# Kernel optimization log

Measured on AMD Instinct MI355X. Metric: run time of the kernel, lower is better.

## Reference

```python
import jax, jax.numpy as jnp
import numpy as np

SQN = 3      # hardcoded recurrence depth
ATT_H = 256  # hardcoded attention hidden size
STRIDE = 16  # segment length (hardcoded expand(-1,16,-1))


def setup_inputs() -> dict:
    key = jax.random.key(0)
    ks = jax.random.split(key, 12)
    B, Cin, H, V = 64, 512, 512, 512

    def w(k, shape, fan_in):
        return jax.random.normal(k, shape, jnp.float32) / np.sqrt(fan_in).astype(np.float32)

    return {
        "visual_input": jax.random.normal(ks[0], (B, Cin, V), jnp.float32),
        "text_feature": jax.random.normal(ks[1], (B, H), jnp.float32),
        # weights stored [in, out] (transposed vs torch nn.Linear)
        "vis_conv_w": w(ks[2], (Cin, H), Cin),   # 1x1 Conv1d == linear over channels
        "vis_conv_b": jnp.zeros((H,), jnp.float32),
        "glob_w": w(ks[3], (SQN, H, H), H),      # 3 distinct global_emb linears
        "glob_b": jnp.zeros((SQN, H), jnp.float32),
        "guide_w": w(ks[4], (2 * H, H), 2 * H),
        "guide_b": jnp.zeros((H,), jnp.float32),
        "att1_w": w(ks[5], (H, ATT_H), H),
        "att1_b": jnp.zeros((ATT_H,), jnp.float32),
        "att2_w": w(ks[6], (H, ATT_H), H),
        "att2_b": jnp.zeros((ATT_H,), jnp.float32),
        "att3_w": w(ks[7], (ATT_H, 1), ATT_H),
        "att3_b": jnp.zeros((1,), jnp.float32),
        "out_conv_w": w(ks[8], (H, H), H),       # 1x1 Conv1d
        "out_conv_b": jnp.zeros((H,), jnp.float32),
        "text_w": w(ks[9], (H, H), H),
        "text_b": jnp.zeros((H,), jnp.float32),
    }


def reference(visual_input, text_feature, vis_conv_w, vis_conv_b, glob_w, glob_b,
              guide_w, guide_b, att1_w, att1_b, att2_w, att2_b, att3_w, att3_b,
              out_conv_w, out_conv_b, text_w, text_b):
    B, Cin, V = visual_input.shape
    H = vis_conv_w.shape[1]
    S = V // STRIDE  # number of segments

    # vis_conv (1x1) + relu: [B, H, V]
    vis_h = jax.nn.relu(jnp.einsum('bcv,ch->bhv', visual_input, vis_conv_w)
                        + vis_conv_b[None, :, None])
    # split into segments: [B, S, T=16, H]
    vis_seg = vis_h.reshape(B, H, S, STRIDE).transpose(0, 2, 3, 1)
    # AvgPool1d(kernel=stride) == per-segment mean: [B, S, H]
    avg_seg = vis_seg.mean(axis=2)
    # text projection: [B, H]
    text_att = text_feature @ text_w + text_b

    # precompute att_fn2(vis_seg): [B, S, T, ATT_H] (loop-invariant)
    att2_pre = jnp.einsum('bsth,ha->bsta', vis_seg, att2_w) + att2_b

    prev_se = jnp.zeros((B, S, H), vis_seg.dtype)
    se_list, att_list = [], []
    for m in range(SQN):  # fixed 3-step recurrence, distinct weights per step
        v_n = jnp.einsum('bsh,hk->bsk', avg_seg, glob_w[m]) + glob_b[m]
        # guide_emb (Linear+ReLU) followed by an outer relu == single relu
        g_n = jax.nn.relu(jnp.concatenate([v_n, prev_se], axis=-1) @ guide_w + guide_b)
        att = jnp.tanh((g_n @ att1_w + att1_b)[:, :, None, :] + att2_pre)  # [B,S,T,A]
        att = att @ att3_w + att3_b                                        # [B,S,T,1]
        att = jax.nn.softmax(att, axis=2)  # softmax over the 16 frames
        prev_se = jnp.sum(vis_seg * att, axis=2)  # [B, S, H]
        se_list.append(prev_se)
        att_list.append(att)

    vis_for_att = jnp.stack(se_list, axis=2)  # [B, S, 3, H]
    fuse_att = jax.nn.softmax(jnp.einsum('bsmh,bh->bsm', vis_for_att, text_att), axis=2)
    vis_new = jnp.einsum('bsmh,bsm->bsh', vis_for_att, fuse_att)  # [B, S, H]

    # vis_out_conv (1x1) + relu over stacked segments: [B, H, S]
    vis_out = jax.nn.relu(jnp.einsum('bsh,hk->bks', vis_new, out_conv_w)
                          + out_conv_b[None, :, None])
    att_out = jnp.concatenate(att_list, axis=3)  # [B, S, 16, 3]
    return vis_out, att_out
```

## Files before the change

### kernel.cpp

```cpp
#include <hip/hip_runtime.h>

#define B_   64
#define CIN_ 512
#define H_   512
#define V_   512
#define S_   32
#define T_   16
#define A_   256
#define SQN_ 3
#define BS_  2048

typedef float  f32x4  __attribute__((ext_vector_type(4)));
typedef float  f32x2  __attribute__((ext_vector_type(2)));
typedef short  short8 __attribute__((ext_vector_type(8)));
typedef short  short4v __attribute__((ext_vector_type(4)));
typedef unsigned int uint4v __attribute__((ext_vector_type(4)));

__device__ __forceinline__ unsigned short f2bf(float f) {
    union { float f; unsigned int u; } v; v.f = f;
    unsigned int u = v.u;
    unsigned int r = (u + 0x7fffu + ((u >> 16) & 1u)) >> 16;
    return (unsigned short)r;
}
__device__ __forceinline__ float bf2f(unsigned short h) {
    union { unsigned int u; float f; } v; v.u = ((unsigned int)h) << 16;
    return v.f;
}

__device__ __forceinline__ float fast_tanhf(float x) {
    float cx = fminf(fmaxf(x, -15.0f), 15.0f);
    float e  = __expf(2.0f * cx);
    return (e - 1.0f) * __builtin_amdgcn_rcpf(e + 1.0f);
}

__device__ __forceinline__ void gload16(const void* g, void* l) {
    __builtin_amdgcn_global_load_lds(
        (const __attribute__((address_space(1))) unsigned int*)g,
        (__attribute__((address_space(3))) unsigned int*)l,
        16, 0, 0);
}

template <int N> __device__ __forceinline__ void waitv() {
    asm volatile("s_waitcnt vmcnt(%0)" :: "n"(N) : "memory");
}

__global__ __launch_bounds__(256) void prep_kernel(
    const float* __restrict__ visual, const float* __restrict__ vis_conv_w,
    const float* __restrict__ att2_w, const float* __restrict__ guide_w,
    const float* __restrict__ att1_w, const float* __restrict__ out_conv_w,
    const float* __restrict__ glob_w, const float* __restrict__ text_feature,
    const float* __restrict__ text_w, const float* __restrict__ text_b,
    const float* __restrict__ glob_b, const float* __restrict__ guide_b,
    unsigned short* __restrict__ visT, unsigned short* __restrict__ wT_visconv,
    unsigned short* __restrict__ wT_att2, unsigned short* __restrict__ wT_guide,
    unsigned short* __restrict__ wT_att1, unsigned short* __restrict__ wT_out,
    unsigned short* __restrict__ glob_bf, float* __restrict__ text_part,
    float* __restrict__ bcomb)
{
    __shared__ __align__(16) char smem[32768];
    const int id  = blockIdx.x;
    const int tid = threadIdx.x;

    if (id < 128) {
        const int nt = id & 7, kc = id >> 3;
        const int n0 = nt * 64, kbase = kc * 32;
        float* Ts = (float*)smem;
        float* Ws = (float*)smem + 64 * 33;
        {
            const int m = tid >> 2, kk = (tid & 3) * 8;
            #pragma unroll
            for (int c = 0; c < 8; c += 4)
                *(f32x4*)&Ts[m * 33 + kk + c] =
                    *(const f32x4*)&text_feature[m * 512 + kbase + kk + c];
            const int kr = tid >> 3, nn = (tid & 7) * 8;
            #pragma unroll
            for (int c = 0; c < 8; c += 4)
                *(f32x4*)&Ws[kr * 65 + nn + c] =
                    *(const f32x4*)&text_w[(long long)(kbase + kr) * 512 + n0 + nn + c];
        }
        __syncthreads();
        const int tm = (tid >> 4) * 4, tn = (tid & 15) * 4;
        float acc[4][4] = {};
        for (int k = 0; k < 32; k++) {
            float a[4], b2[4];
            #pragma unroll
            for (int i = 0; i < 4; i++) a[i] = Ts[(tm + i) * 33 + k];
            #pragma unroll
            for (int j = 0; j < 4; j++) b2[j] = Ws[k * 65 + tn + j];
            #pragma unroll
            for (int i = 0; i < 4; i++)
                #pragma unroll
                for (int j = 0; j < 4; j++) acc[i][j] += a[i] * b2[j];
        }
        #pragma unroll
        for (int i = 0; i < 4; i++)
            #pragma unroll
            for (int j = 0; j < 4; j++)
                text_part[kc * (64 * 512) + (tm + i) * 512 + n0 + tn + j] =
                    acc[i][j] + (kc == 0 ? text_b[n0 + tn + j] : 0.0f);
        return;
    }
    if (id < 131) {
        const int m = id - 128;
        const int j2 = tid * 2;
        float a0 = guide_b[j2], a1 = guide_b[j2 + 1];
        const float* gb = glob_b + m * 512;
        #pragma unroll 8
        for (int k = 0; k < 512; k++) {
            const float g = gb[k];
            f32x2 w = *(const f32x2*)&guide_w[(long long)k * 512 + j2];
            a0 += g * w[0];
            a1 += g * w[1];
        }
        f32x2 o = {a0, a1};
        *(f32x2*)&bcomb[m * 512 + j2] = o;
        return;
    }
    if (id < 227) {
        const int base = (id - 131) * 8192 + tid * 4;
        #pragma unroll
        for (int it = 0; it < 8; it++) {
            f32x4 v = *(const f32x4*)&glob_w[base + it * 1024];
            short4v o;
            #pragma unroll
            for (int c = 0; c < 4; c++) o[c] = (short)f2bf(v[c]);
            *(short4v*)&glob_bf[base + it * 1024] = o;
        }
        return;
    }

    if (id >= 547) {
        const int q = id - 547;
        const int b = q >> 5, tile = q & 31;
        const int k0 = (tile >> 2) << 6;
        const int v0 = (tile & 3) << 7;
        const float* src = visual + (long long)b * 262144;
        unsigned short* dst = visT + (long long)b * 262144;
        float* tl = (float*)smem;

        const int wave = tid >> 6, lane = tid & 63;
        #pragma unroll
        for (int i = 0; i < 8; i++) {
            const int r2 = wave * 16 + i * 2;
            gload16(&src[(long long)(k0 + r2 + (lane >> 5)) * 512 + v0 + (lane & 31) * 4],
                    &tl[r2 * 128]);
        }
        __syncthreads();

        const int kl = (tid & 7) * 8;
        const int vb = tid >> 3;
        #pragma unroll
        for (int jv = 0; jv < 4; jv++) {
            const int v = vb + jv * 32;
            short8 o;
            #pragma unroll
            for (int i = 0; i < 8; i++)
                o[i] = (short)f2bf(tl[(kl + i) * 128 + v]);
            *(short8*)&dst[(long long)(v0 + v) * 512 + k0 + kl] = o;
        }
        return;
    }

    const float* src; unsigned short* dst; int Kd, Nd, tile;
    if (id < 291)      { tile = id - 227; src = vis_conv_w; dst = wT_visconv; Kd = 512;  Nd = 512; }
    else if (id < 323) { tile = id - 291; src = att2_w;     dst = wT_att2;    Kd = 512;  Nd = 256; }
    else if (id < 451) { tile = id - 323; src = guide_w;    dst = wT_guide;   Kd = 1024; Nd = 512; }
    else if (id < 483) { tile = id - 451; src = att1_w;     dst = wT_att1;    Kd = 512;  Nd = 256; }
    else               { tile = id - 483; src = out_conv_w; dst = wT_out;     Kd = 512;  Nd = 512; }

    unsigned int* tl = (unsigned int*)smem;
    const int xw = Nd >> 6;
    const int n0 = (tile % xw) << 6, k0 = (tile / xw) << 6;
    {
        const int r = tid >> 4;
        const int c4 = (tid & 15) * 4;
        #pragma unroll
        for (int j = 0; j < 4; j++) {
            const int row = j * 16 + r;
            f32x4 v = *(const f32x4*)&src[(long long)(k0 + row) * Nd + n0 + c4];
            #pragma unroll
            for (int c2 = 0; c2 < 4; c2++)
                tl[row * 65 + c4 + c2] = f2bf(v[c2]);
        }
    }
    __syncthreads();
    {
        const int v = tid >> 2, cq = (tid & 3) * 16;
        short8 o0, o1;
        #pragma unroll
        for (int j = 0; j < 8; j++) o0[j] = (short)tl[(cq + j) * 65 + v];
        #pragma unroll
        for (int j = 0; j < 8; j++) o1[j] = (short)tl[(cq + 8 + j) * 65 + v];
        *(short8*)&dst[(long long)(n0 + v) * Kd + k0 + cq] = o0;
        *(short8*)&dst[(long long)(n0 + v) * Kd + k0 + cq + 8] = o1;
    }
}

template <int BM, int BN, bool RELU, bool OUT_BF16, int OUT_MODE, bool ACC_INIT, int DEPTH>
__device__ __forceinline__ void gemm_body(
    char* pool, int bid, int nwg,
    const unsigned short* __restrict__ A, long long aBatch, int lda,
    const unsigned short* __restrict__ Bt, long long bBatch, int ldb,
    const float* __restrict__ bias, long long biasBatch,
    const float* __restrict__ Cinit, int ldci,
    void* __restrict__ C, long long cBatch, int ldc,
    void* __restrict__ C2, unsigned short* __restrict__ avg_out,
    int M, int N, int K)
{
    constexpr int WM = BM / 2, WN = BN / 2;
    constexpr int FI = WM / 16, FJ = WN / 16;
    constexpr int LOADS = BM / 64 + BN / 64;
    constexpr bool CT_EN  = (OUT_MODE != 1);
    constexpr bool CT_F32 = CT_EN && ((OUT_MODE == 0 && !OUT_BF16) || OUT_MODE == 3);
    constexpr int  CTS    = CT_F32 ? (BN + 4) : (BN + 8);
    constexpr int  KLOOP_B = DEPTH * (BM * 32 + BN * 32) * 2;
    constexpr int  CT_B    = CT_EN ? (BM * CTS * (CT_F32 ? 4 : 2)) : 0;
    constexpr int  MAIN_B  = (KLOOP_B > CT_B ? KLOOP_B : CT_B);
    unsigned short* As = (unsigned short*)pool;
    unsigned short* Bs = As + DEPTH * BM * 32;
    float* avgl = (float*)(pool + MAIN_B);

    const int q8 = nwg >> 3, r8 = nwg & 7;
    const int xcd = bid & 7, lid = bid >> 3;
    const int logical = (xcd < r8 ? xcd * (q8 + 1)
                                  : r8 * (q8 + 1) + (xcd - r8) * q8) + lid;

    const int ntiles = N / BN;
    const int tilesPerBatch = (M / BM) * ntiles;
    const int batch = logical / tilesPerBatch;
    const int t     = logical % tilesPerBatch;
    const int tm0 = (t / ntiles) * BM;
    const int tn0 = (t % ntiles) * BN;
    const unsigned short* Ab = A + (long long)batch * aBatch;
    const unsigned short* Bb = Bt + (long long)batch * bBatch;

    const int tid  = threadIdx.x;
    const int lane = tid & 63;
    const int wave = tid >> 6;
    const int wm = (wave >> 1) * WM;
    const int wn = (wave & 1) * WN;
    const int lr = lane & 15;
    const int lk = (lane >> 4) * 8;
    const int rsub = lane >> 2;
    const int g8s = ((lane & 3) ^ ((lane >> 3) & 3)) * 8;
    const int lks = lk ^ (((lr >> 1) & 3) << 3);

    auto stage = [&](int buf, int k0) {
        #pragma unroll
        for (int i = 0; i < BM / 64; i++) {
            const int rbase = wave * (BM / 4) + i * 16;
            gload16(&Ab[(long long)(tm0 + rbase + rsub) * lda + k0 + g8s],
                    &As[buf * (BM * 32) + rbase * 32]);
        }
        #pragma unroll
        for (int i = 0; i < BN / 64; i++) {
            const int rbase = wave * (BN / 4) + i * 16;
            gload16(&Bb[(long long)(tn0 + rbase + rsub) * ldb + k0 + g8s],
                    &Bs[buf * (BN * 32) + rbase * 32]);
        }
    };

    f32x4 acc[FI][FJ] = {};
    const int nk = K >> 5;

    #pragma unroll
    for (int d = 0; d < DEPTH - 1; d++)
        if (d < nk) stage(d, d << 5);

    int cur = 0;
    for (int kt = 0; kt < nk; kt++) {
        if (kt + DEPTH - 1 < nk) {
            const int nb = cur + DEPTH - 1;
            stage(nb >= DEPTH ? nb - DEPTH : nb, (kt + DEPTH - 1) << 5);
        }
        if constexpr (DEPTH == 2) {
            if (kt + 1 < nk) waitv<LOADS>(); else waitv<0>();
        } else {
            if (kt + 2 < nk)      waitv<2 * LOADS>();
            else if (kt + 1 < nk) waitv<LOADS>();
            else                  waitv<0>();
        }
        __builtin_amdgcn_s_barrier();

        const unsigned short* Ac = As + cur * (BM * 32);
        const unsigned short* Bc = Bs + cur * (BN * 32);
        short8 a[FI], b[FJ];
        #pragma unroll
        for (int i = 0; i < FI; i++)
            a[i] = *(const short8*)&Ac[(wm + i * 16 + lr) * 32 + lks];
        #pragma unroll
        for (int j = 0; j < FJ; j++)
            b[j] = *(const short8*)&Bc[(wn + j * 16 + lr) * 32 + lks];
        #pragma unroll
        for (int i = 0; i < FI; i++)
            #pragma unroll
            for (int j = 0; j < FJ; j++)
                acc[i][j] = __builtin_amdgcn_mfma_f32_16x16x32_bf16(
                    a[i], b[j], acc[i][j], 0, 0, 0);
        __builtin_amdgcn_sched_barrier(0);
        __builtin_amdgcn_s_barrier();
        cur = (cur + 1 == DEPTH) ? 0 : cur + 1;
    }

    const int erow = (lane >> 4) * 4;
    const int ecol = lane & 15;

    if constexpr (OUT_MODE == 1) {
        #pragma unroll
        for (int i = 0; i < FI; i++) {
            #pragma unroll
            for (int j = 0; j < FJ; j++) {
                const int gcol = tn0 + wn + j * 16 + ecol;
                const float bv = bias ? bias[gcol] : 0.0f;
                const int grow0 = tm0 + wm + i * 16 + erow;
                const int bb = grow0 >> 5, ss = grow0 & 31;
                f32x4 o;
                #pragma unroll
                for (int r = 0; r < 4; r++) o[r] = fmaxf(acc[i][j][r] + bv, 0.0f);
                *(f32x4*)&((float*)C)[(long long)bb * (H_ * S_) + gcol * S_ + ss] = o;
            }
        }
        return;
    } else {
        __syncthreads();
        unsigned short* CTh = (unsigned short*)pool;
        float*          CTf = (float*)pool;

        #pragma unroll
        for (int i = 0; i < FI; i++) {
            #pragma unroll
            for (int j = 0; j < FJ; j++) {
                const int lcol = wn + j * 16 + ecol;
                const int gcol = tn0 + lcol;
                const float bv = bias ? bias[(long long)batch * biasBatch + gcol] : 0.0f;
                float csum = 0.0f;
                #pragma unroll
                for (int r = 0; r < 4; r++) {
                    const int lrow = wm + i * 16 + erow + r;
                    float v = acc[i][j][r] + bv;
                    if (ACC_INIT) v += Cinit[(long long)(tm0 + lrow) * ldci + gcol];
                    if (RELU) v = fmaxf(v, 0.0f);
                    if constexpr (CT_F32) CTf[lrow * CTS + lcol] = v;
                    else                  CTh[lrow * CTS + lcol] = f2bf(v);
                    if constexpr (OUT_MODE == 2) csum += v;
                }
                if constexpr (OUT_MODE == 2) {
                    csum += __shfl_xor(csum, 16, 64);
                    csum += __shfl_xor(csum, 32, 64);
                    if (lane < 16)
                        avgl[((wm >> 4) + i) * BN + wn + j * 16 + lane] = csum;
                }
            }
        }
        __syncthreads();

        if constexpr (CT_F32) {
            constexpr int ITERS = (BM * BN) / 1024;
            #pragma unroll
            for (int it = 0; it < ITERS; it++) {
                const int flat = it * 1024 + tid * 4;
                const int row = flat / BN, col = flat % BN;
                f32x4 vv = *(const f32x4*)&CTf[row * CTS + col];
                if constexpr (OUT_MODE == 3) {
                    if (batch == 0) {
                        short4v p;
                        #pragma unroll
                        for (int c = 0; c < 4; c++) p[c] = (short)f2bf(fmaxf(vv[c], 0.0f));
                        *(short4v*)&((unsigned short*)C2)[(long long)(tm0 + row) * ldc + tn0 + col] = p;
                    } else {
                        *(f32x4*)&((float*)C)[(long long)(batch - 1) * cBatch +
                                              (long long)(tm0 + row) * ldc + tn0 + col] = vv;
                    }
                } else {
                    *(f32x4*)&((float*)C)[(long long)batch * cBatch +
                                          (long long)(tm0 + row) * ldc + tn0 + col] = vv;
                }
            }
        } else {
            constexpr int ITERS = (BM * BN) / 2048;
            #pragma unroll
            for (int it = 0; it < ITERS; it++) {
                const int flat = it * 2048 + tid * 8;
                const int row = flat / BN, col = flat % BN;
                short8 vv = *(const short8*)&CTh[row * CTS + col];
                *(short8*)&((unsigned short*)C)[(long long)batch * cBatch +
                                                (long long)(tm0 + row) * ldc + tn0 + col] = vv;
            }
        }

        if constexpr (OUT_MODE == 2) {
            const int s = tid >> 5, hq = (tid & 31) * 4;
            short4v pk;
            #pragma unroll
            for (int c = 0; c < 4; c++)
                pk[c] = (short)f2bf(avgl[s * BN + hq + c] * (1.0f / 16.0f));
            *(short4v*)&avg_out[((long long)batch * 32 + (tm0 >> 4) + s) * H_ + tn0 + hq] = pk;
        }
    }
}

__device__ __forceinline__ void visconv_pair_body(
    char* pool, int bid, int nwg,
    const unsigned short* __restrict__ visT,
    const unsigned short* __restrict__ Bw,
    const float* __restrict__ bias,
    unsigned short* __restrict__ vis_seg,
    unsigned short* __restrict__ avg_out)
{
    unsigned short* As = (unsigned short*)pool;
    unsigned short* Bs = As + 16384;
    float* avgl = (float*)(pool + 49152);

    const int logical = (bid & 7) * (nwg >> 3) + (bid >> 3);
    const int pairIdx = logical >> 4;
    const int t = logical & 15;
    const int tm0 = (t >> 2) * 128, tn0 = (t & 3) * 128;
    const int b0 = pairIdx * 2;
    const unsigned short* A0 = visT + (long long)b0 * (V_ * CIN_);
    const unsigned short* A1 = A0 + V_ * CIN_;

    const int tid  = threadIdx.x;
    const int lane = tid & 63, wave = tid >> 6;
    const int wm = (wave >> 1) * 64, wn = (wave & 1) * 64;
    const int lr = lane & 15, lk = (lane >> 4) * 8;
    const int rsub = lane >> 2;
    const int g8s = ((lane & 3) ^ ((lane >> 3) & 3)) * 8;
    const int lks = lk ^ (((lr >> 1) & 3) << 3);

    auto stage = [&](int buf, int k0) {
        #pragma unroll
        for (int i = 0; i < 2; i++) {
            const int rbase = wave * 32 + i * 16;
            gload16(&A0[(long long)(tm0 + rbase + rsub) * CIN_ + k0 + g8s],
                    &As[(0 + buf) * 4096 + rbase * 32]);
            gload16(&A1[(long long)(tm0 + rbase + rsub) * CIN_ + k0 + g8s],
                    &As[(2 + buf) * 4096 + rbase * 32]);
            gload16(&Bw[(long long)(tn0 + rbase + rsub) * CIN_ + k0 + g8s],
                    &Bs[buf * 4096 + rbase * 32]);
        }
    };

    f32x4 acc0[4][4] = {}, acc1[4][4] = {};

    stage(0, 0);
    int cur = 0;
    for (int kt = 0; kt < 16; kt++) {
        if (kt + 1 < 16) stage(cur ^ 1, (kt + 1) << 5);
        if (kt + 1 < 16) waitv<6>(); else waitv<0>();
        __builtin_amdgcn_s_barrier();

        const unsigned short* Bc = Bs + cur * 4096;
        short8 b[4];
        #pragma unroll
        for (int j = 0; j < 4; j++)
            b[j] = *(const short8*)&Bc[(wn + j * 16 + lr) * 32 + lks];
        {
            const unsigned short* Ac = As + cur * 4096;
            short8 a[4];
            #pragma unroll
            for (int i = 0; i < 4; i++)
                a[i] = *(const short8*)&Ac[(wm + i * 16 + lr) * 32 + lks];
            #pragma unroll
            for (int i = 0; i < 4; i++)
                #pragma unroll
                for (int j = 0; j < 4; j++)
                    acc0[i][j] = __builtin_amdgcn_mfma_f32_16x16x32_bf16(
                        a[i], b[j], acc0[i][j], 0, 0, 0);
        }
        {
            const unsigned short* Ac = As + (2 + cur) * 4096;
            short8 a[4];
            #pragma unroll
            for (int i = 0; i < 4; i++)
                a[i] = *(const short8*)&Ac[(wm + i * 16 + lr) * 32 + lks];
            #pragma unroll
            for (int i = 0; i < 4; i++)
                #pragma unroll
                for (int j = 0; j < 4; j++)
                    acc1[i][j] = __builtin_amdgcn_mfma_f32_16x16x32_bf16(
                        a[i], b[j], acc1[i][j], 0, 0, 0);
        }
        __builtin_amdgcn_sched_barrier(0);
        __builtin_amdgcn_s_barrier();
        cur ^= 1;
    }

    const int erow = (lane >> 4) * 4;
    const int ecol = lane & 15;
    unsigned short* CTh = (unsigned short*)pool;

    auto epil = [&](f32x4 (&acc)[4][4], int b) {
        #pragma unroll
        for (int i = 0; i < 4; i++) {
            #pragma unroll
            for (int j = 0; j < 4; j++) {
                const int lcol = wn + j * 16 + ecol;
                const float bv = bias[tn0 + lcol];
                float csum = 0.0f;
                #pragma unroll
                for (int r = 0; r < 4; r++) {
                    const int lrow = wm + i * 16 + erow + r;
                    float v = fmaxf(acc[i][j][r] + bv, 0.0f);
                    CTh[lrow * 136 + lcol] = f2bf(v);
                    csum += v;
                }
                csum += __shfl_xor(csum, 16, 64);
                csum += __shfl_xor(csum, 32, 64);
                if (lane < 16)
                    avgl[((wm >> 4) + i) * 128 + wn + j * 16 + lane] = csum;
            }
        }
        __syncthreads();
        #pragma unroll
        for (int it = 0; it < 8; it++) {
            const int flat = it * 2048 + tid * 8;
            const int row = flat >> 7, col = flat & 127;
            short8 vv = *(const short8*)&CTh[row * 136 + col];
            *(short8*)&vis_seg[(long long)b * (V_ * H_) +
                               (long long)(tm0 + row) * H_ + tn0 + col] = vv;
        }
        {
            const int s = tid >> 5, hq = (tid & 31) * 4;
            short4v pk;
            #pragma unroll
            for (int c = 0; c < 4; c++)
                pk[c] = (short)f2bf(avgl[s * 128 + hq + c] * (1.0f / 16.0f));
            *(short4v*)&avg_out[((long long)b * 32 + (tm0 >> 4) + s) * H_ + tn0 + hq] = pk;
        }
        __syncthreads();
    };
    epil(acc0, b0);
    epil(acc1, b0 + 1);
}

template <int BM, int BN, bool RELU, bool OUT_BF16, int OUT_MODE, bool ACC_INIT, int DEPTH>
__global__ __launch_bounds__(256) void mfma_gemm(
    const unsigned short* A, long long aBatch, int lda,
    const unsigned short* Bt, long long bBatch, int ldb,
    const float* bias, long long biasBatch,
    const float* Cinit, int ldci,
    void* C, long long cBatch, int ldc,
    void* C2, unsigned short* avg_out,
    int M, int N, int K)
{
    constexpr bool CT_EN  = (OUT_MODE != 1);
    constexpr bool CT_F32 = CT_EN && ((OUT_MODE == 0 && !OUT_BF16) || OUT_MODE == 3);
    constexpr int  CTS    = CT_F32 ? (BN + 4) : (BN + 8);
    constexpr int  KLOOP_B = DEPTH * (BM * 32 + BN * 32) * 2;
    constexpr int  CT_B    = CT_EN ? (BM * CTS * (CT_F32 ? 4 : 2)) : 0;
    constexpr int  MAIN_B  = (KLOOP_B > CT_B ? KLOOP_B : CT_B);
    constexpr int  AVG_B   = (OUT_MODE == 2) ? (BM / 16) * BN * 4 : 0;
    __shared__ __align__(16) char pool[MAIN_B + AVG_B];
    gemm_body<BM, BN, RELU, OUT_BF16, OUT_MODE, ACC_INIT, DEPTH>(
        pool, blockIdx.x, gridDim.x,
        A, aBatch, lda, Bt, bBatch, ldb, bias, biasBatch, Cinit, ldci,
        C, cBatch, ldc, C2, avg_out, M, N, K);
}

__global__ __launch_bounds__(256) void wcomb_visconv_kernel(
    const unsigned short* wT_guide, const unsigned short* glob_bf,
    unsigned short* WcombT,
    const unsigned short* visT, const unsigned short* wT_visconv,
    const float* vis_conv_b, unsigned short* vis_seg, unsigned short* avg)
{
    __shared__ __align__(16) char pool[53248];
    if (blockIdx.x < 192) {
        gemm_body<64, 64, false, true, 0, false, 2>(pool, blockIdx.x, 192,
            wT_guide, 0, 1024,
            glob_bf, (long long)H_ * H_, H_,
            nullptr, 0, nullptr, 0,
            WcombT, (long long)H_ * H_, H_, nullptr, nullptr, H_, H_, H_);
    } else {
        visconv_pair_body(pool, blockIdx.x - 192, 512,
            visT, wT_visconv, vis_conv_b, vis_seg, avg);
    }
}

__global__ __launch_bounds__(256) void att2_p_kernel(
    const unsigned short* vis_seg, const unsigned short* wT_att2,
    const float* att2_b, unsigned short* att2_pre,
    const unsigned short* avg, const unsigned short* WcombT,
    const float* bcomb, float* P, unsigned short* gbuf)
{
    __shared__ __align__(16) char pool[34816];
    if (blockIdx.x < 512) {
        gemm_body<128, 128, false, true, 0, false, 2>(pool, blockIdx.x, 512,
            vis_seg, (long long)V_ * H_, H_,
            wT_att2, 0, H_,
            att2_b, 0, nullptr, 0,
            att2_pre, (long long)V_ * A_, A_, nullptr, nullptr, V_, A_, H_);
    } else {
        gemm_body<64, 64, false, false, 3, false, 2>(pool, blockIdx.x - 512, 768,
            avg, 0, H_,
            WcombT, (long long)H_ * H_, H_,
            bcomb, H_, nullptr, 0,
            P, (long long)BS_ * H_, H_, gbuf, nullptr, BS_, H_, H_);
    }
}

template <bool LAST>
__global__ __launch_bounds__(256) void fused_att_kernel(
    const float* __restrict__ att1,
    const unsigned short* __restrict__ att2_pre,
    const float* __restrict__ att3_w,
    const float* __restrict__ att3_b,
    const unsigned short* __restrict__ vis_seg,
    float* __restrict__ se_m,
    unsigned short* __restrict__ pse,
    float* __restrict__ att_out, int m,
    const float* __restrict__ se_base,
    const float* __restrict__ text_part,
    const float* __restrict__ text_b,
    unsigned short* __restrict__ vis_new)
{
    const int bs = blockIdx.x, tid = threadIdx.x;
    const int wave = tid >> 6, lane = tid & 63;
    __shared__ float logits[T_], wts[T_];
    __shared__ float part[3][512];
    __shared__ float redf[4][3];
    __shared__ float swf[3];
    __shared__ float tsh[512];

    if constexpr (LAST) {
        const int b = bs >> 5;
        for (int h = tid; h < 512; h += 256) {
            float s = text_b[h];
            #pragma unroll
            for (int p = 0; p < 16; p++)
                s += text_part[p * (64 * 512) + b * 512 + h];
            tsh[h] = s;
        }
    }

    f32x4 a1r = *(const f32x4*)&att1[(long long)bs * A_ + lane * 4];
    f32x4 w3r = *(const f32x4*)&att3_w[lane * 4];

    #pragma unroll
    for (int qq = 0; qq < 4; qq++) {
        const int t = wave * 4 + qq;
        short4v ap = *(const short4v*)&att2_pre[(long long)(bs * T_ + t) * A_ + lane * 4];
        float x = 0.f;
        #pragma unroll
        for (int c = 0; c < 4; c++)
            x += fast_tanhf(a1r[c] + bf2f((unsigned short)ap[c])) * w3r[c];
        #pragma unroll
        for (int off = 32; off > 0; off >>= 1) x += __shfl_down(x, off, 64);
        if (lane == 0) logits[t] = x + att3_b[0];
    }
    __syncthreads();
    if (tid == 0) {
        float mx = logits[0];
        #pragma unroll
        for (int t = 1; t < T_; t++) mx = fmaxf(mx, logits[t]);
        float s = 0.f;
        #pragma unroll
        for (int t = 0; t < T_; t++) { float e = expf(logits[t] - mx); wts[t] = e; s += e; }
        float inv = 1.0f / s;
        #pragma unroll
        for (int t = 0; t < T_; t++) wts[t] *= inv;
    }
    __syncthreads();
    if (tid < T_) att_out[bs * (T_ * SQN_) + tid * SQN_ + m] = wts[tid];

    const int slot = tid & 63, quarter = tid >> 6;
    float s[8] = {};
    #pragma unroll
    for (int tt = 0; tt < 4; tt++) {
        const int t = quarter * 4 + tt;
        short8 vv = *(const short8*)&vis_seg[(long long)(bs * T_ + t) * H_ + slot * 8];
        const float w = wts[t];
        #pragma unroll
        for (int c = 0; c < 8; c++) s[c] += bf2f((unsigned short)vv[c]) * w;
    }
    if (quarter) {
        #pragma unroll
        for (int c = 0; c < 8; c++) part[quarter - 1][slot * 8 + c] = s[c];
    }
    __syncthreads();
    if (quarter == 0) {
        #pragma unroll
        for (int c = 0; c < 8; c++)
            s[c] += part[0][slot * 8 + c] + part[1][slot * 8 + c] + part[2][slot * 8 + c];
    }

    if constexpr (!LAST) {
        if (quarter == 0) {
            f32x4 o0 = {s[0], s[1], s[2], s[3]};
            f32x4 o1 = {s[4], s[5], s[6], s[7]};
            *(f32x4*)&se_m[(long long)bs * H_ + slot * 8] = o0;
            *(f32x4*)&se_m[(long long)bs * H_ + slot * 8 + 4] = o1;
            short8 p;
            #pragma unroll
            for (int c = 0; c < 8; c++) p[c] = (short)f2bf(s[c]);
            *(short8*)&pse[(long long)bs * H_ + slot * 8] = p;
        }
    } else {
        const float* se0 = se_base + (long long)bs * H_;
        const float* se1 = se_base + (long long)BS_ * H_ + (long long)bs * H_;

        float p0 = 0.f, p1 = 0.f, p2 = 0.f;
        {
            const int h2 = tid * 2;
            float t0 = tsh[h2], t1 = tsh[h2 + 1];
            p0 = se0[h2] * t0 + se0[h2 + 1] * t1;
            p1 = se1[h2] * t0 + se1[h2 + 1] * t1;
        }
        if (quarter == 0) {
            #pragma unroll
            for (int c = 0; c < 8; c++) p2 += s[c] * tsh[slot * 8 + c];
        }
        #pragma unroll
        for (int off = 32; off > 0; off >>= 1) {
            p0 += __shfl_down(p0, off, 64);
            p1 += __shfl_down(p1, off, 64);
            p2 += __shfl_down(p2, off, 64);
        }
        if (lane == 0) { redf[wave][0] = p0; redf[wave][1] = p1; redf[wave][2] = p2; }
        __syncthreads();
        if (tid == 0) {
            float d0 = redf[0][0] + redf[1][0] + redf[2][0] + redf[3][0];
            float d1 = redf[0][1] + redf[1][1] + redf[2][1] + redf[3][1];
            float d2 = redf[0][2] + redf[1][2] + redf[2][2] + redf[3][2];
            float mx = fmaxf(d0, fmaxf(d1, d2));
            float e0 = expf(d0 - mx), e1 = expf(d1 - mx), e2 = expf(d2 - mx);
            float inv = 1.0f / (e0 + e1 + e2);
            swf[0] = e0 * inv; swf[1] = e1 * inv; swf[2] = e2 * inv;
        }
        __syncthreads();
        if (quarter == 0) {
            const float w0 = swf[0], w1 = swf[1], w2 = swf[2];
            short8 p;
            #pragma unroll
            for (int c = 0; c < 8; c++) {
                const int h = slot * 8 + c;
                p[c] = (short)f2bf(w0 * se0[h] + w1 * se1[h] + w2 * s[c]);
            }
            *(short8*)&vis_new[(long long)bs * H_ + slot * 8] = p;
        }
    }
}

extern "C" void kernel_launch(void* const* d_in, const int* in_sizes, int n_in,
                              void* d_out, int out_size, void* d_ws, size_t ws_size,
                              hipStream_t stream)
{
    const float* visual       = (const float*)d_in[0];
    const float* text_feature = (const float*)d_in[1];
    const float* vis_conv_w   = (const float*)d_in[2];
    const float* vis_conv_b   = (const float*)d_in[3];
    const float* glob_w       = (const float*)d_in[4];
    const float* glob_b       = (const float*)d_in[5];
    const float* guide_w      = (const float*)d_in[6];
    const float* guide_b      = (const float*)d_in[7];
    const float* att1_w       = (const float*)d_in[8];
    const float* att1_b       = (const float*)d_in[9];
    const float* att2_w       = (const float*)d_in[10];
    const float* att2_b       = (const float*)d_in[11];
    const float* att3_w       = (const float*)d_in[12];
    const float* att3_b       = (const float*)d_in[13];
    const float* out_conv_w   = (const float*)d_in[14];
    const float* out_conv_b   = (const float*)d_in[15];
    const float* text_w       = (const float*)d_in[16];
    const float* text_b       = (const float*)d_in[17];
    float* out = (float*)d_out;
    float* att_out = out + (B_ * H_ * S_);

    char* base = (char*)d_ws;
    unsigned short* visT     = (unsigned short*)(base + 0);
    unsigned short* vis_seg  = (unsigned short*)(base + 33554432);
    unsigned short* att2_pre = (unsigned short*)(base + 67108864);
    float*          se       = (float*)(base + 100663296);
    float*          P        = (float*)(base + 113246208);
    unsigned short* pse      = (unsigned short*)(base + 125829120);
    unsigned short* gbuf     = (unsigned short*)(base + 127926272);
    float*          att1buf  = (float*)(base + 130023424);
    unsigned short* avg      = (unsigned short*)(base + 132120576);
    unsigned short* vis_new  = (unsigned short*)(base + 134348800);
    char*           wbase    = base + 136445952;
    unsigned short* wT_visconv = (unsigned short*)(wbase + 0);
    unsigned short* wT_att2    = (unsigned short*)(wbase + 524288);
    unsigned short* wT_guide   = (unsigned short*)(wbase + 786432);
    unsigned short* wT_att1    = (unsigned short*)(wbase + 1835008);
    unsigned short* wT_out     = (unsigned short*)(wbase + 2097152);
    unsigned short* glob_bf    = (unsigned short*)(wbase + 2621440);
    unsigned short* WcombT     = (unsigned short*)(wbase + 4194304);
    float*          bcomb      = (float*)(wbase + 5767168);
    float*          text_part  = (float*)(wbase + 6291456);

    prep_kernel<<<dim3(2595), 256, 0, stream>>>(
        visual, vis_conv_w, att2_w, guide_w, att1_w, out_conv_w, glob_w,
        text_feature, text_w, text_b, glob_b, guide_b,
        visT, wT_visconv, wT_att2, wT_guide, wT_att1, wT_out,
        glob_bf, text_part, bcomb);

    wcomb_visconv_kernel<<<dim3(192 + 512), 256, 0, stream>>>(
        wT_guide, glob_bf, WcombT,
        visT, wT_visconv, vis_conv_b, vis_seg, avg);

    att2_p_kernel<<<dim3(512 + 768), 256, 0, stream>>>(
        vis_seg, wT_att2, att2_b, att2_pre,
        avg, WcombT, bcomb, P, gbuf);

    for (int m = 0; m < SQN_; m++) {
        if (m > 0) {
            mfma_gemm<64, 64, true, true, 0, true, 3><<<dim3(256), 256, 0, stream>>>(
                pse, 0, H_,
                wT_guide + 512, 0, 1024,
                nullptr, 0, P + (long long)(m - 1) * BS_ * H_, H_,
                gbuf, 0, H_, nullptr, nullptr, BS_, H_, H_);
        }
        mfma_gemm<64, 64, false, false, 0, false, 3><<<dim3(128), 256, 0, stream>>>(
            gbuf, 0, H_,
            wT_att1, 0, H_,
            att1_b, 0, nullptr, 0,
            att1buf, 0, A_, nullptr, nullptr, BS_, A_, H_);
        if (m < SQN_ - 1) {
            fused_att_kernel<false><<<dim3(BS_), 256, 0, stream>>>(
                att1buf, att2_pre, att3_w, att3_b, vis_seg,
                se + (long long)m * BS_ * H_, pse, att_out, m,
                nullptr, nullptr, nullptr, nullptr);
        } else {
            fused_att_kernel<true><<<dim3(BS_), 256, 0, stream>>>(
                att1buf, att2_pre, att3_w, att3_b, vis_seg,
                nullptr, nullptr, att_out, m,
                se, text_part, text_b, vis_new);
        }
    }

    mfma_gemm<64, 64, true, false, 1, false, 3><<<dim3(256), 256, 0, stream>>>(
        vis_new, 0, H_,
        wT_out, 0, H_,
        out_conv_b, 0, nullptr, 0,
        out, 0, 0, nullptr, nullptr, BS_, H_, H_);
}
```

Baseline: 164.8 us.

## Fuse visual input transpose and bf16 cast into vis_conv GEMM A-loading

Drops the prep-kernel pass that transposed the fp32 visual input into a bf16 visT buffer. The vis_conv GEMM now stages fp32 tiles of the visual input straight into LDS, using an XOR swizzle, and converts them to bf16 when building the MFMA A fragments. Each block now handles one batch instead of a pair, so the grid doubles and the shared B tile is no longer reused across two batches. This removes a 64MB read and 32MB write round trip, but the GEMM now reads fp32 A (twice the bytes), does scalar strided LDS reads, and spends extra ALU on conversion in the inner loop.

Measured after the change: 176.5 us. 7.1% more time.

```diff
diff --git a/kernel.cpp b/kernel.cpp
--- a/kernel.cpp
+++ b/kernel.cpp
@@ -45,13 +45,13 @@
 }
 
 __global__ __launch_bounds__(256) void prep_kernel(
-    const float* __restrict__ visual, const float* __restrict__ vis_conv_w,
+    const float* __restrict__ vis_conv_w,
     const float* __restrict__ att2_w, const float* __restrict__ guide_w,
     const float* __restrict__ att1_w, const float* __restrict__ out_conv_w,
     const float* __restrict__ glob_w, const float* __restrict__ text_feature,
     const float* __restrict__ text_w, const float* __restrict__ text_b,
     const float* __restrict__ glob_b, const float* __restrict__ guide_b,
-    unsigned short* __restrict__ visT, unsigned short* __restrict__ wT_visconv,
+    unsigned short* __restrict__ wT_visconv,
     unsigned short* __restrict__ wT_att2, unsigned short* __restrict__ wT_guide,
     unsigned short* __restrict__ wT_att1, unsigned short* __restrict__ wT_out,
     unsigned short* __restrict__ glob_bf, float* __restrict__ text_part,
@@ -125,38 +125,6 @@
             #pragma unroll
             for (int c = 0; c < 4; c++) o[c] = (short)f2bf(v[c]);
             *(short4v*)&glob_bf[base + it * 1024] = o;
-        }
-        return;
-    }
-
-    if (id >= 547) {
-        const int q = id - 547;
-        const int b = q >> 5, tile = q & 31;
-        const int k0 = (tile >> 2) << 6;
-        const int v0 = (tile & 3) << 7;
-        const float* src = visual + (long long)b * 262144;
-        unsigned short* dst = visT + (long long)b * 262144;
-        float* tl = (float*)smem;
-
-        const int wave = tid >> 6, lane = tid & 63;
-        #pragma unroll
-        for (int i = 0; i < 8; i++) {
-            const int r2 = wave * 16 + i * 2;
-            gload16(&src[(long long)(k0 + r2 + (lane >> 5)) * 512 + v0 + (lane & 31) * 4],
-                    &tl[r2 * 128]);
-        }
-        __syncthreads();
-
-        const int kl = (tid & 7) * 8;
-        const int vb = tid >> 3;
-        #pragma unroll
-        for (int jv = 0; jv < 4; jv++) {
-            const int v = vb + jv * 32;
-            short8 o;
-            #pragma unroll
-            for (int i = 0; i < 8; i++)
-                o[i] = (short)f2bf(tl[(kl + i) * 128 + v]);
-            *(short8*)&dst[(long long)(v0 + v) * 512 + k0 + kl] = o;
         }
         return;
     }
@@ -399,49 +367,49 @@
     }
 }
 
-__device__ __forceinline__ void visconv_pair_body(
+__device__ __forceinline__ void visconv_f32_body(
     char* pool, int bid, int nwg,
-    const unsigned short* __restrict__ visT,
+    const float* __restrict__ visual,
     const unsigned short* __restrict__ Bw,
     const float* __restrict__ bias,
     unsigned short* __restrict__ vis_seg,
     unsigned short* __restrict__ avg_out)
 {
-    unsigned short* As = (unsigned short*)pool;
-    unsigned short* Bs = As + 16384;
-    float* avgl = (float*)(pool + 49152);
+    float*          Asf = (float*)pool;
+    unsigned short* Bs  = (unsigned short*)(pool + 32768);
+    float*          avgl = (float*)(pool + 49152);
 
     const int logical = (bid & 7) * (nwg >> 3) + (bid >> 3);
-    const int pairIdx = logical >> 4;
+    const int b = logical >> 4;
     const int t = logical & 15;
-    const int tm0 = (t >> 2) * 128, tn0 = (t & 3) * 128;
-    const int b0 = pairIdx * 2;
-    const unsigned short* A0 = visT + (long long)b0 * (V_ * CIN_);
-    const unsigned short* A1 = A0 + V_ * CIN_;
-
-    const int tid  = threadIdx.x;
-    const int lane = tid & 63, wave = tid >> 6;
+    const int tm0 = (t >> 2) * 128;
+    const int tn0 = (t & 3) * 128;
+    const float* Ab = visual + (long long)b * (CIN_ * V_);
+
+    const int tid = threadIdx.x, lane = tid & 63, wave = tid >> 6;
     const int wm = (wave >> 1) * 64, wn = (wave & 1) * 64;
     const int lr = lane & 15, lk = (lane >> 4) * 8;
     const int rsub = lane >> 2;
     const int g8s = ((lane & 3) ^ ((lane >> 3) & 3)) * 8;
     const int lks = lk ^ (((lr >> 1) & 3) << 3);
+    const int vsrc = ((lane & 31) * 4) ^ ((wave & 1) << 4);
+    const int akey = ((lane >> 4) & 1) << 4;
 
     auto stage = [&](int buf, int k0) {
+        #pragma unroll
+        for (int i = 0; i < 4; i++) {
+            gload16(&Ab[(long long)(k0 + wave * 8 + i * 2 + (lane >> 5)) * V_ + tm0 + vsrc],
+                    (char*)Asf + buf * 16384 + (wave * 8 + i * 2) * 512);
+        }
         #pragma unroll
         for (int i = 0; i < 2; i++) {
             const int rbase = wave * 32 + i * 16;
-            gload16(&A0[(long long)(tm0 + rbase + rsub) * CIN_ + k0 + g8s],
-                    &As[(0 + buf) * 4096 + rbase * 32]);
-            gload16(&A1[(long long)(tm0 + rbase + rsub) * CIN_ + k0 + g8s],
-                    &As[(2 + buf) * 4096 + rbase * 32]);
             gload16(&Bw[(long long)(tn0 + rbase + rsub) * CIN_ + k0 + g8s],
-                    &Bs[buf * 4096 + rbase * 32]);
+                    (char*)Bs + buf * 8192 + rbase * 64);
         }
     };
 
-    f32x4 acc0[4][4] = {}, acc1[4][4] = {};
-
+    f32x4 acc[4][4] = {};
     stage(0, 0);
     int cur = 0;
     for (int kt = 0; kt < 16; kt++) {
@@ -449,37 +417,27 @@
         if (kt + 1 < 16) waitv<6>(); else waitv<0>();
         __builtin_amdgcn_s_barrier();
 
-        const unsigned short* Bc = Bs + cur * 4096;
-        short8 b[4];
+        const float*          Ac = Asf + cur * 4096;
+        const unsigned short* Bc = Bs  + cur * 4096;
+        short8 a[4], bfr[4];
         #pragma unroll
         for (int j = 0; j < 4; j++)
-            b[j] = *(const short8*)&Bc[(wn + j * 16 + lr) * 32 + lks];
-        {
-            const unsigned short* Ac = As + cur * 4096;
-            short8 a[4];
-            #pragma unroll
-            for (int i = 0; i < 4; i++)
-                a[i] = *(const short8*)&Ac[(wm + i * 16 + lr) * 32 + lks];
-            #pragma unroll
-            for (int i = 0; i < 4; i++)
-                #pragma unroll
-                for (int j = 0; j < 4; j++)
-                    acc0[i][j] = __builtin_amdgcn_mfma_f32_16x16x32_bf16(
-                        a[i], b[j], acc0[i][j], 0, 0, 0);
-        }
-        {
-            const unsigned short* Ac = As + (2 + cur) * 4096;
-            short8 a[4];
-            #pragma unroll
-            for (int i = 0; i < 4; i++)
-                a[i] = *(const short8*)&Ac[(wm + i * 16 + lr) * 32 + lks];
-            #pragma unroll
-            for (int i = 0; i < 4; i++)
-                #pragma unroll
-                for (int j = 0; j < 4; j++)
-                    acc1[i][j] = __builtin_amdgcn_mfma_f32_16x16x32_bf16(
-                        a[i], b[j], acc1[i][j], 0, 0, 0);
-        }
+            bfr[j] = *(const short8*)&Bc[(wn + j * 16 + lr) * 32 + lks];
+        #pragma unroll
+        for (int i = 0; i < 4; i++) {
+            const int vx = (wm + i * 16 + lr) ^ akey;
+            short8 av;
+            #pragma unroll
+            for (int e = 0; e < 8; e++)
+                av[e] = (short)f2bf(Ac[(lk + e) * 128 + vx]);
+            a[i] = av;
+        }
+        #pragma unroll
+        for (int i = 0; i < 4; i++)
+            #pragma unroll
+            for (int j = 0; j < 4; j++)
+                acc[i][j] = __builtin_amdgcn_mfma_f32_16x16x32_bf16(
+                    a[i], bfr[j], acc[i][j], 0, 0, 0);
         __builtin_amdgcn_sched_barrier(0);
         __builtin_amdgcn_s_barrier();
         cur ^= 1;
@@ -488,49 +446,45 @@
     const int erow = (lane >> 4) * 4;
     const int ecol = lane & 15;
     unsigned short* CTh = (unsigned short*)pool;
-
-    auto epil = [&](f32x4 (&acc)[4][4], int b) {
-        #pragma unroll
-        for (int i = 0; i < 4; i++) {
-            #pragma unroll
-            for (int j = 0; j < 4; j++) {
-                const int lcol = wn + j * 16 + ecol;
-                const float bv = bias[tn0 + lcol];
-                float csum = 0.0f;
-                #pragma unroll
-                for (int r = 0; r < 4; r++) {
-                    const int lrow = wm + i * 16 + erow + r;
-                    float v = fmaxf(acc[i][j][r] + bv, 0.0f);
-                    CTh[lrow * 136 + lcol] = f2bf(v);
-                    csum += v;
-                }
-                csum += __shfl_xor(csum, 16, 64);
-                csum += __shfl_xor(csum, 32, 64);
-                if (lane < 16)
-                    avgl[((wm >> 4) + i) * 128 + wn + j * 16 + lane] = csum;
+    __syncthreads();
+
+    #pragma unroll
+    for (int i = 0; i < 4; i++) {
+        #pragma unroll
+        for (int j = 0; j < 4; j++) {
+            const int lcol = wn + j * 16 + ecol;
+            const float bv = bias[tn0 + lcol];
+            float csum = 0.0f;
+            #pragma unroll
+            for (int r = 0; r < 4; r++) {
+                const int lrow = wm + i * 16 + erow + r;
+                float v = fmaxf(acc[i][j][r] + bv, 0.0f);
+                CTh[lrow * 136 + lcol] = f2bf(v);
+                csum += v;
             }
-        }
-        __syncthreads();
-        #pragma unroll
-        for (int it = 0; it < 8; it++) {
-            const int flat = it * 2048 + tid * 8;
-            const int row = flat >> 7, col = flat & 127;
-            short8 vv = *(const short8*)&CTh[row * 136 + col];
-            *(short8*)&vis_seg[(long long)b * (V_ * H_) +
-                               (long long)(tm0 + row) * H_ + tn0 + col] = vv;
-        }
-        {
-            const int s = tid >> 5, hq = (tid & 31) * 4;
-            short4v pk;
-            #pragma unroll
-            for (int c = 0; c < 4; c++)
-                pk[c] = (short)f2bf(avgl[s * 128 + hq + c] * (1.0f / 16.0f));
-            *(short4v*)&avg_out[((long long)b * 32 + (tm0 >> 4) + s) * H_ + tn0 + hq] = pk;
-        }
-        __syncthreads();
-    };
-    epil(acc0, b0);
-    epil(acc1, b0 + 1);
+            csum += __shfl_xor(csum, 16, 64);
+            csum += __shfl_xor(csum, 32, 64);
+            if (lane < 16)
+                avgl[((wm >> 4) + i) * 128 + wn + j * 16 + lane] = csum;
+        }
+    }
+    __syncthreads();
+    #pragma unroll
+    for (int it = 0; it < 8; it++) {
+        const int flat = it * 2048 + tid * 8;
+        const int row = flat >> 7, col = flat & 127;
+        short8 vv = *(const short8*)&CTh[row * 136 + col];
+        *(short8*)&vis_seg[(long long)b * (V_ * H_) +
+                           (long long)(tm0 + row) * H_ + tn0 + col] = vv;
+    }
+    {
+        const int s = tid >> 5, hq = (tid & 31) * 4;
+        short4v pk;
+        #pragma unroll
+        for (int c = 0; c < 4; c++)
+            pk[c] = (short)f2bf(avgl[s * 128 + hq + c] * (1.0f / 16.0f));
+        *(short4v*)&avg_out[((long long)b * 32 + (tm0 >> 4) + s) * H_ + tn0 + hq] = pk;
+    }
 }
 
 template <int BM, int BN, bool RELU, bool OUT_BF16, int OUT_MODE, bool ACC_INIT, int DEPTH>
@@ -560,7 +514,7 @@
 __global__ __launch_bounds__(256) void wcomb_visconv_kernel(
     const unsigned short* wT_guide, const unsigned short* glob_bf,
     unsigned short* WcombT,
-    const unsigned short* visT, const unsigned short* wT_visconv,
+    const float* visual, const unsigned short* wT_visconv,
     const float* vis_conv_b, unsigned short* vis_seg, unsigned short* avg)
 {
     __shared__ __align__(16) char pool[53248];
@@ -571,8 +525,8 @@
             nullptr, 0, nullptr, 0,
             WcombT, (long long)H_ * H_, H_, nullptr, nullptr, H_, H_, H_);
     } else {
-        visconv_pair_body(pool, blockIdx.x - 192, 512,
-            visT, wT_visconv, vis_conv_b, vis_seg, avg);
+        visconv_f32_body(pool, blockIdx.x - 192, 1024,
+            visual, wT_visconv, vis_conv_b, vis_seg, avg);
     }
 }
 
@@ -766,7 +720,6 @@
     float* att_out = out + (B_ * H_ * S_);
 
     char* base = (char*)d_ws;
-    unsigned short* visT     = (unsigned short*)(base + 0);
     unsigned short* vis_seg  = (unsigned short*)(base + 33554432);
     unsigned short* att2_pre = (unsigned short*)(base + 67108864);
     float*          se       = (float*)(base + 100663296);
@@ -787,15 +740,15 @@
     float*          bcomb      = (float*)(wbase + 5767168);
     float*          text_part  = (float*)(wbase + 6291456);
 
-    prep_kernel<<<dim3(2595), 256, 0, stream>>>(
-        visual, vis_conv_w, att2_w, guide_w, att1_w, out_conv_w, glob_w,
+    prep_kernel<<<dim3(547), 256, 0, stream>>>(
+        vis_conv_w, att2_w, guide_w, att1_w, out_conv_w, glob_w,
         text_feature, text_w, text_b, glob_b, guide_b,
-        visT, wT_visconv, wT_att2, wT_guide, wT_att1, wT_out,
+        wT_visconv, wT_att2, wT_guide, wT_att1, wT_out,
         glob_bf, text_part, bcomb);
 
-    wcomb_visconv_kernel<<<dim3(192 + 512), 256, 0, stream>>>(
+    wcomb_visconv_kernel<<<dim3(192 + 1024), 256, 0, stream>>>(
         wT_guide, glob_bf, WcombT,
-        visT, wT_visconv, vis_conv_b, vis_seg, avg);
+        visual, wT_visconv, vis_conv_b, vis_seg, avg);
 
     att2_p_kernel<<<dim3(512 + 768), 256, 0, stream>>>(
         vis_seg, wT_att2, att2_b, att2_pre,
```
